# Kernel tuning notes

Measured on AMD Instinct MI355X. Metric: run time of the kernel, lower is better.

The kernel has to match this reference:

```python
import jax, jax.numpy as jnp
import numpy as np

EPS = 1e-6

def _feature_map(x):
    # elu(x) + 1  (positive feature map)
    return jax.nn.elu(x) + 1.0

def setup_inputs() -> dict:
    key = jax.random.key(0)
    k1, k2, k3 = jax.random.split(key, 3)
    B, N, H, D = 4, 4096, 8, 64
    M = 64
    return {
        "queries": jax.random.normal(k1, (B, N, H, D), dtype=jnp.float32),
        "keys": jax.random.normal(k2, (B, N, H, D), dtype=jnp.float32),
        "values": jax.random.normal(k3, (B, N, H, M), dtype=jnp.float32),
        "attn_mask": jnp.zeros((1,), dtype=bool),
    }

def reference(queries, keys, values, attn_mask):
    Q = _feature_map(queries)            # [b,n,h,d]
    K = _feature_map(keys)               # [b,n,h,d]
    KV = jnp.einsum('bnhd,bnhm->bhmd', K, values)          # [b,h,m,d]
    K_sum = K.sum(axis=1)                                  # [b,h,d]
    Z = 1.0 / (jnp.einsum('bnhd,bhd->bnh', Q, K_sum) + EPS)  # [b,n,h]
    V = jnp.einsum('bnhd,bhmd,bnh->bnhm', Q, KV, Z)        # [b,n,h,m]
    return V
```

## Files before the change

kernel.cpp:

```cpp
#include <hip/hip_runtime.h>


#define EPSC 1e-6f

constexpr int Bq = 4;
constexpr int Nq = 4096;
constexpr int Hq = 8;
constexpr int Dq = 64;
constexpr int Mq = 64;
constexpr int BH = Bq * Hq;
constexpr int RSTR = Hq * Dq;
constexpr int TILESZ = Mq * Dq;

__device__ __forceinline__ float fmap(float x) {
    return x > 0.0f ? x + 1.0f : __expf(x);
}

__global__ __launch_bounds__(256)
void phase1_kv(const float* __restrict__ Kp, const float* __restrict__ Vp,
               float* __restrict__ partKV, float* __restrict__ partKS)
{
    const int wid  = threadIdx.x >> 6;
    const int lane = threadIdx.x & 63;
    const int tile = blockIdx.x * 4 + wid;
    const int bh = blockIdx.x >> 4;
    const int ck = blockIdx.x & 15;
    const int b  = bh >> 3;
    const int h  = bh & 7;
    const int dg = lane & 7;
    const int mg = lane >> 3;
    const int n0base = ck * 256 + wid * 64;

    const float* Kb = Kp + (size_t)(b * Nq + n0base) * RSTR + h * Dq;
    const float* Vb = Vp + (size_t)(b * Nq + n0base) * RSTR + h * Dq;

    float acc[8][8];
    #pragma unroll
    for (int i = 0; i < 8; ++i)
        #pragma unroll
        for (int j = 0; j < 8; ++j) acc[i][j] = 0.0f;
    float ksum[8] = {0.f,0.f,0.f,0.f,0.f,0.f,0.f,0.f};

    #pragma unroll 2
    for (int n0 = 0; n0 < 64; n0 += 4) {
        float4 kA[4], kB[4], vA[4], vB[4];
        #pragma unroll
        for (int u = 0; u < 4; ++u) {
            const float* kr = Kb + (size_t)(n0 + u) * RSTR;
            const float* vr = Vb + (size_t)(n0 + u) * RSTR;
            kA[u] = *(const float4*)(kr + dg * 8);
            kB[u] = *(const float4*)(kr + dg * 8 + 4);
            vA[u] = *(const float4*)(vr + mg * 8);
            vB[u] = *(const float4*)(vr + mg * 8 + 4);
        }
        #pragma unroll
        for (int u = 0; u < 4; ++u) {
            float kf[8], vf[8];
            kf[0] = fmap(kA[u].x); kf[1] = fmap(kA[u].y); kf[2] = fmap(kA[u].z); kf[3] = fmap(kA[u].w);
            kf[4] = fmap(kB[u].x); kf[5] = fmap(kB[u].y); kf[6] = fmap(kB[u].z); kf[7] = fmap(kB[u].w);
            vf[0] = vA[u].x; vf[1] = vA[u].y; vf[2] = vA[u].z; vf[3] = vA[u].w;
            vf[4] = vB[u].x; vf[5] = vB[u].y; vf[6] = vB[u].z; vf[7] = vB[u].w;
            #pragma unroll
            for (int mi = 0; mi < 8; ++mi)
                #pragma unroll
                for (int di = 0; di < 8; ++di)
                    acc[mi][di] = fmaf(vf[mi], kf[di], acc[mi][di]);
            if (mg == 0) {
                #pragma unroll
                for (int di = 0; di < 8; ++di) ksum[di] += kf[di];
            }
        }
    }

    float* dst = partKV + (size_t)tile * TILESZ;
    #pragma unroll
    for (int mi = 0; mi < 8; ++mi) {
        const int m = mg * 8 + mi;
        float4 a0 = make_float4(acc[mi][0], acc[mi][1], acc[mi][2], acc[mi][3]);
        float4 a1 = make_float4(acc[mi][4], acc[mi][5], acc[mi][6], acc[mi][7]);
        *(float4*)&dst[m * Dq + dg * 8]     = a0;
        *(float4*)&dst[m * Dq + dg * 8 + 4] = a1;
    }
    if (mg == 0) {
        float* kd = partKS + (size_t)tile * Dq + dg * 8;
        *(float4*)&kd[0] = make_float4(ksum[0], ksum[1], ksum[2], ksum[3]);
        *(float4*)&kd[4] = make_float4(ksum[4], ksum[5], ksum[6], ksum[7]);
    }
}

__global__ __launch_bounds__(256)
void phase1b_reduce(const float* __restrict__ partKV, const float* __restrict__ partKS,
                    float* __restrict__ KV, float* __restrict__ KS)
{
    const int bh = blockIdx.x >> 2;
    const int q  = blockIdx.x & 3;
    const int t  = threadIdx.x;
    const int off = q * 1024 + t * 4;
    const float* src = partKV + (size_t)bh * 64 * TILESZ;

    float4 a = make_float4(0.f, 0.f, 0.f, 0.f);
    #pragma unroll 8
    for (int p = 0; p < 64; ++p) {
        float4 v = *(const float4*)(src + (size_t)p * TILESZ + off);
        a.x += v.x; a.y += v.y; a.z += v.z; a.w += v.w;
    }
    *(float4*)&KV[(size_t)bh * TILESZ + off] = a;

    if (q == 0 && t < Dq) {
        const float* ks = partKS + (size_t)bh * 64 * Dq;
        float s = 0.0f;
        #pragma unroll 8
        for (int p = 0; p < 64; ++p) s += ks[p * Dq + t];
        KS[bh * Dq + t] = s;
    }
}

constexpr int RC2 = 256;

__global__ __launch_bounds__(256, 2)
void phase2_out(const float* __restrict__ Qp, const float* __restrict__ wsKV,
                const float* __restrict__ wsKS, float* __restrict__ Out)
{
    constexpr int CH = Nq / RC2;
    const int bh = blockIdx.x / CH;
    const int ck = blockIdx.x - bh * CH;
    const int b  = bh >> 3;
    const int h  = bh & 7;

    __shared__ float sKV[Mq * 68];
    __shared__ float sKS[Dq];

    const int tid = threadIdx.x;
    const float* kvsrc = wsKV + (size_t)bh * TILESZ;
    #pragma unroll
    for (int it = 0; it < 4; ++it) {
        const int flat = tid * 4 + it * 1024;
        const int m = flat >> 6, d = flat & 63;
        *(float4*)&sKV[m * 68 + d] = *(const float4*)(kvsrc + flat);
    }
    if (tid < 16) {
        *(float4*)&sKS[tid * 4] = *(const float4*)(wsKS + bh * Dq + tid * 4);
    }
    __syncthreads();

    const int mg = tid & 7;
    const int rg = tid >> 3;
    const int row0 = ck * RC2 + rg * 8;
    const float* Qb = Qp + (size_t)(b * Nq + row0) * RSTR + h * Dq;

    float acc[8][8];
    float zac[8];
    #pragma unroll
    for (int i = 0; i < 8; ++i) {
        zac[i] = 0.0f;
        #pragma unroll
        for (int j = 0; j < 8; ++j) acc[i][j] = 0.0f;
    }

    #pragma unroll 2
    for (int d4 = 0; d4 < 16; ++d4) {
        const float4 ks4 = *(const float4*)&sKS[d4 * 4];
        float qf[8][4];
        #pragma unroll
        for (int i = 0; i < 8; ++i) {
            const float4 q = *(const float4*)(Qb + (size_t)i * RSTR + d4 * 4);
            qf[i][0] = fmap(q.x); qf[i][1] = fmap(q.y);
            qf[i][2] = fmap(q.z); qf[i][3] = fmap(q.w);
            zac[i] = fmaf(qf[i][0], ks4.x, zac[i]);
            zac[i] = fmaf(qf[i][1], ks4.y, zac[i]);
            zac[i] = fmaf(qf[i][2], ks4.z, zac[i]);
            zac[i] = fmaf(qf[i][3], ks4.w, zac[i]);
        }
        #pragma unroll
        for (int mi = 0; mi < 8; ++mi) {
            const float4 kv4 = *(const float4*)&sKV[(mg + 8 * mi) * 68 + d4 * 4];
            #pragma unroll
            for (int i = 0; i < 8; ++i) {
                acc[i][mi] = fmaf(qf[i][0], kv4.x, acc[i][mi]);
                acc[i][mi] = fmaf(qf[i][1], kv4.y, acc[i][mi]);
                acc[i][mi] = fmaf(qf[i][2], kv4.z, acc[i][mi]);
                acc[i][mi] = fmaf(qf[i][3], kv4.w, acc[i][mi]);
            }
        }
    }

    float* Ob = Out + (size_t)(b * Nq + row0) * RSTR + h * Mq;
    #pragma unroll
    for (int i = 0; i < 8; ++i) {
        const float z = 1.0f / (zac[i] + EPSC);
        #pragma unroll
        for (int mi = 0; mi < 8; ++mi)
            Ob[(size_t)i * RSTR + mg + 8 * mi] = acc[i][mi] * z;
    }
}

extern "C" void kernel_launch(void* const* d_in, const int* in_sizes, int n_in,
                              void* d_out, int out_size, void* d_ws, size_t ws_size,
                              hipStream_t stream)
{
    (void)in_sizes; (void)n_in; (void)out_size; (void)ws_size;
    const float* Q = (const float*)d_in[0];
    const float* K = (const float*)d_in[1];
    const float* V = (const float*)d_in[2];
    float* out = (float*)d_out;

    float* partKV = out;
    float* wsKV   = (float*)d_ws;
    float* wsKS   = wsKV + (size_t)BH * TILESZ;
    float* partKS = wsKS + (size_t)BH * Dq;

    phase1_kv<<<BH * 16, 256, 0, stream>>>(K, V, partKV, partKS);
    phase1b_reduce<<<BH * 4, 256, 0, stream>>>(partKV, partKS, wsKV, wsKS);
    phase2_out<<<BH * (Nq / RC2), 256, 0, stream>>>(Q, wsKV, wsKS, out);
}
```

Baseline: 243.6 us.

## Restructure all three kernels with new thread mappings and finer partitioning

```diff
diff --git a/kernel.cpp b/kernel.cpp
--- a/kernel.cpp
+++ b/kernel.cpp
@@ -20,177 +20,153 @@
 void phase1_kv(const float* __restrict__ Kp, const float* __restrict__ Vp,
                float* __restrict__ partKV, float* __restrict__ partKS)
 {
-    const int wid  = threadIdx.x >> 6;
+    const int t  = blockIdx.x;
+    const int bh = t >> 6, ck = t & 63;
+    const int b  = bh >> 3, h = bh & 7;
+    const int w    = threadIdx.x >> 6;
     const int lane = threadIdx.x & 63;
-    const int tile = blockIdx.x * 4 + wid;
-    const int bh = blockIdx.x >> 4;
-    const int ck = blockIdx.x & 15;
-    const int b  = bh >> 3;
-    const int h  = bh & 7;
-    const int dg = lane & 7;
-    const int mg = lane >> 3;
-    const int n0base = ck * 256 + wid * 64;
+    const int m0   = w * 16;
 
-    const float* Kb = Kp + (size_t)(b * Nq + n0base) * RSTR + h * Dq;
-    const float* Vb = Vp + (size_t)(b * Nq + n0base) * RSTR + h * Dq;
+    const float* Kb = Kp + ((size_t)(b * Nq + ck * 64) * Hq + h) * Dq;
+    const float* Vb = Vp + ((size_t)(b * Nq + ck * 64) * Hq + h) * Mq;
 
-    float acc[8][8];
+    float acc[16];
     #pragma unroll
-    for (int i = 0; i < 8; ++i)
-        #pragma unroll
-        for (int j = 0; j < 8; ++j) acc[i][j] = 0.0f;
-    float ksum[8] = {0.f,0.f,0.f,0.f,0.f,0.f,0.f,0.f};
+    for (int i = 0; i < 16; ++i) acc[i] = 0.0f;
+    float ksum = 0.0f;
 
     #pragma unroll 2
-    for (int n0 = 0; n0 < 64; n0 += 4) {
-        float4 kA[4], kB[4], vA[4], vB[4];
+    for (int n = 0; n < 64; n += 2) {
+        const float k0 = Kb[(size_t)n * RSTR + lane];
+        const float k1 = Kb[(size_t)(n + 1) * RSTR + lane];
+        const float* v0 = Vb + (size_t)n * RSTR + m0;
+        const float* v1 = Vb + (size_t)(n + 1) * RSTR + m0;
+        float4 va[4], vb[4];
         #pragma unroll
-        for (int u = 0; u < 4; ++u) {
-            const float* kr = Kb + (size_t)(n0 + u) * RSTR;
-            const float* vr = Vb + (size_t)(n0 + u) * RSTR;
-            kA[u] = *(const float4*)(kr + dg * 8);
-            kB[u] = *(const float4*)(kr + dg * 8 + 4);
-            vA[u] = *(const float4*)(vr + mg * 8);
-            vB[u] = *(const float4*)(vr + mg * 8 + 4);
+        for (int j = 0; j < 4; ++j) {
+            va[j] = *(const float4*)(v0 + j * 4);
+            vb[j] = *(const float4*)(v1 + j * 4);
         }
+        const float kf0 = fmap(k0);
+        const float kf1 = fmap(k1);
+        ksum += kf0 + kf1;
         #pragma unroll
-        for (int u = 0; u < 4; ++u) {
-            float kf[8], vf[8];
-            kf[0] = fmap(kA[u].x); kf[1] = fmap(kA[u].y); kf[2] = fmap(kA[u].z); kf[3] = fmap(kA[u].w);
-            kf[4] = fmap(kB[u].x); kf[5] = fmap(kB[u].y); kf[6] = fmap(kB[u].z); kf[7] = fmap(kB[u].w);
-            vf[0] = vA[u].x; vf[1] = vA[u].y; vf[2] = vA[u].z; vf[3] = vA[u].w;
-            vf[4] = vB[u].x; vf[5] = vB[u].y; vf[6] = vB[u].z; vf[7] = vB[u].w;
-            #pragma unroll
-            for (int mi = 0; mi < 8; ++mi)
-                #pragma unroll
-                for (int di = 0; di < 8; ++di)
-                    acc[mi][di] = fmaf(vf[mi], kf[di], acc[mi][di]);
-            if (mg == 0) {
-                #pragma unroll
-                for (int di = 0; di < 8; ++di) ksum[di] += kf[di];
-            }
+        for (int j = 0; j < 4; ++j) {
+            acc[j*4+0] = fmaf(kf0, va[j].x, acc[j*4+0]);
+            acc[j*4+1] = fmaf(kf0, va[j].y, acc[j*4+1]);
+            acc[j*4+2] = fmaf(kf0, va[j].z, acc[j*4+2]);
+            acc[j*4+3] = fmaf(kf0, va[j].w, acc[j*4+3]);
+            acc[j*4+0] = fmaf(kf1, vb[j].x, acc[j*4+0]);
+            acc[j*4+1] = fmaf(kf1, vb[j].y, acc[j*4+1]);
+            acc[j*4+2] = fmaf(kf1, vb[j].z, acc[j*4+2]);
+            acc[j*4+3] = fmaf(kf1, vb[j].w, acc[j*4+3]);
         }
     }
 
-    float* dst = partKV + (size_t)tile * TILESZ;
+    float* dst = partKV + (size_t)t * TILESZ;
     #pragma unroll
-    for (int mi = 0; mi < 8; ++mi) {
-        const int m = mg * 8 + mi;
-        float4 a0 = make_float4(acc[mi][0], acc[mi][1], acc[mi][2], acc[mi][3]);
-        float4 a1 = make_float4(acc[mi][4], acc[mi][5], acc[mi][6], acc[mi][7]);
-        *(float4*)&dst[m * Dq + dg * 8]     = a0;
-        *(float4*)&dst[m * Dq + dg * 8 + 4] = a1;
-    }
-    if (mg == 0) {
-        float* kd = partKS + (size_t)tile * Dq + dg * 8;
-        *(float4*)&kd[0] = make_float4(ksum[0], ksum[1], ksum[2], ksum[3]);
-        *(float4*)&kd[4] = make_float4(ksum[4], ksum[5], ksum[6], ksum[7]);
-    }
+    for (int mi = 0; mi < 16; ++mi)
+        dst[(m0 + mi) * Dq + lane] = acc[mi];
+    if (w == 0)
+        partKS[(size_t)t * Dq + lane] = ksum;
 }
 
 __global__ __launch_bounds__(256)
 void phase1b_reduce(const float* __restrict__ partKV, const float* __restrict__ partKS,
                     float* __restrict__ KV, float* __restrict__ KS)
 {
-    const int bh = blockIdx.x >> 2;
-    const int q  = blockIdx.x & 3;
-    const int t  = threadIdx.x;
-    const int off = q * 1024 + t * 4;
-    const float* src = partKV + (size_t)bh * 64 * TILESZ;
+    const int bh = blockIdx.x >> 4, six = blockIdx.x & 15;
+    const int f  = threadIdx.x & 63, pg = threadIdx.x >> 6;
+    const size_t base = (size_t)bh * 64 * TILESZ + six * 256 + f * 4;
 
     float4 a = make_float4(0.f, 0.f, 0.f, 0.f);
-    #pragma unroll 8
-    for (int p = 0; p < 64; ++p) {
-        float4 v = *(const float4*)(src + (size_t)p * TILESZ + off);
+    #pragma unroll
+    for (int p = 0; p < 16; ++p) {
+        const float4 v = *(const float4*)(partKV + base + (size_t)(pg * 16 + p) * TILESZ);
         a.x += v.x; a.y += v.y; a.z += v.z; a.w += v.w;
     }
-    *(float4*)&KV[(size_t)bh * TILESZ + off] = a;
 
-    if (q == 0 && t < Dq) {
-        const float* ks = partKS + (size_t)bh * 64 * Dq;
-        float s = 0.0f;
-        #pragma unroll 8
-        for (int p = 0; p < 64; ++p) s += ks[p * Dq + t];
-        KS[bh * Dq + t] = s;
+    float ks = 0.0f;
+    if (six == 0) {
+        #pragma unroll
+        for (int p = 0; p < 16; ++p)
+            ks += partKS[(size_t)(bh * 64 + pg * 16 + p) * Dq + f];
+    }
+
+    __shared__ float4 sred[4][64];
+    __shared__ float  sks[4][64];
+    sred[pg][f] = a;
+    sks[pg][f]  = ks;
+    __syncthreads();
+
+    if (pg == 0) {
+        float4 r  = sred[0][f];
+        const float4 r1 = sred[1][f], r2 = sred[2][f], r3 = sred[3][f];
+        r.x += r1.x + r2.x + r3.x;
+        r.y += r1.y + r2.y + r3.y;
+        r.z += r1.z + r2.z + r3.z;
+        r.w += r1.w + r2.w + r3.w;
+        *(float4*)(KV + (size_t)bh * TILESZ + six * 256 + f * 4) = r;
+        if (six == 0)
+            KS[bh * Dq + f] = sks[0][f] + sks[1][f] + sks[2][f] + sks[3][f];
     }
 }
 
-constexpr int RC2 = 256;
+__global__ __launch_bounds__(256)
+void phase2_out(const float* __restrict__ Qp, const float* __restrict__ KV,
+                const float* __restrict__ KS, float* __restrict__ Out)
+{
+    const int blk = blockIdx.x;
+    const int bh = blk >> 5, ck = blk & 31;
+    const int b  = bh >> 3,  h  = bh & 7;
+    const int mg = threadIdx.x & 7;
+    const int rt = threadIdx.x >> 3;
+    const int row0 = ck * 128 + rt * 4;
 
-__global__ __launch_bounds__(256, 2)
-void phase2_out(const float* __restrict__ Qp, const float* __restrict__ wsKV,
-                const float* __restrict__ wsKS, float* __restrict__ Out)
-{
-    constexpr int CH = Nq / RC2;
-    const int bh = blockIdx.x / CH;
-    const int ck = blockIdx.x - bh * CH;
-    const int b  = bh >> 3;
-    const int h  = bh & 7;
+    const float* Qb  = Qp + ((size_t)(b * Nq + row0) * Hq + h) * Dq;
+    const float* KVb = KV + (size_t)bh * TILESZ + mg * 8 * Dq;
+    const float* KSb = KS + bh * Dq;
 
-    __shared__ float sKV[Mq * 68];
-    __shared__ float sKS[Dq];
-
-    const int tid = threadIdx.x;
-    const float* kvsrc = wsKV + (size_t)bh * TILESZ;
+    float acc[4][8];
+    float zac[4] = {0.f, 0.f, 0.f, 0.f};
     #pragma unroll
-    for (int it = 0; it < 4; ++it) {
-        const int flat = tid * 4 + it * 1024;
-        const int m = flat >> 6, d = flat & 63;
-        *(float4*)&sKV[m * 68 + d] = *(const float4*)(kvsrc + flat);
-    }
-    if (tid < 16) {
-        *(float4*)&sKS[tid * 4] = *(const float4*)(wsKS + bh * Dq + tid * 4);
-    }
-    __syncthreads();
-
-    const int mg = tid & 7;
-    const int rg = tid >> 3;
-    const int row0 = ck * RC2 + rg * 8;
-    const float* Qb = Qp + (size_t)(b * Nq + row0) * RSTR + h * Dq;
-
-    float acc[8][8];
-    float zac[8];
-    #pragma unroll
-    for (int i = 0; i < 8; ++i) {
-        zac[i] = 0.0f;
+    for (int i = 0; i < 4; ++i)
         #pragma unroll
         for (int j = 0; j < 8; ++j) acc[i][j] = 0.0f;
-    }
 
-    #pragma unroll 2
+    #pragma unroll 4
     for (int d4 = 0; d4 < 16; ++d4) {
-        const float4 ks4 = *(const float4*)&sKS[d4 * 4];
-        float qf[8][4];
+        const float4 ks4 = *(const float4*)(KSb + d4 * 4);
+        float4 kv[8];
         #pragma unroll
-        for (int i = 0; i < 8; ++i) {
+        for (int mi = 0; mi < 8; ++mi)
+            kv[mi] = *(const float4*)(KVb + mi * Dq + d4 * 4);
+        #pragma unroll
+        for (int i = 0; i < 4; ++i) {
             const float4 q = *(const float4*)(Qb + (size_t)i * RSTR + d4 * 4);
-            qf[i][0] = fmap(q.x); qf[i][1] = fmap(q.y);
-            qf[i][2] = fmap(q.z); qf[i][3] = fmap(q.w);
-            zac[i] = fmaf(qf[i][0], ks4.x, zac[i]);
-            zac[i] = fmaf(qf[i][1], ks4.y, zac[i]);
-            zac[i] = fmaf(qf[i][2], ks4.z, zac[i]);
-            zac[i] = fmaf(qf[i][3], ks4.w, zac[i]);
-        }
-        #pragma unroll
-        for (int mi = 0; mi < 8; ++mi) {
-            const float4 kv4 = *(const float4*)&sKV[(mg + 8 * mi) * 68 + d4 * 4];
+            const float q0 = fmap(q.x), q1 = fmap(q.y), q2 = fmap(q.z), q3 = fmap(q.w);
+            zac[i] = fmaf(q0, ks4.x, zac[i]);
+            zac[i] = fmaf(q1, ks4.y, zac[i]);
+            zac[i] = fmaf(q2, ks4.z, zac[i]);
+            zac[i] = fmaf(q3, ks4.w, zac[i]);
             #pragma unroll
-            for (int i = 0; i < 8; ++i) {
-                acc[i][mi] = fmaf(qf[i][0], kv4.x, acc[i][mi]);
-                acc[i][mi] = fmaf(qf[i][1], kv4.y, acc[i][mi]);
-                acc[i][mi] = fmaf(qf[i][2], kv4.z, acc[i][mi]);
-                acc[i][mi] = fmaf(qf[i][3], kv4.w, acc[i][mi]);
+            for (int mi = 0; mi < 8; ++mi) {
+                acc[i][mi] = fmaf(q0, kv[mi].x, acc[i][mi]);
+                acc[i][mi] = fmaf(q1, kv[mi].y, acc[i][mi]);
+                acc[i][mi] = fmaf(q2, kv[mi].z, acc[i][mi]);
+                acc[i][mi] = fmaf(q3, kv[mi].w, acc[i][mi]);
             }
         }
     }
 
-    float* Ob = Out + (size_t)(b * Nq + row0) * RSTR + h * Mq;
+    float* Ob = Out + ((size_t)(b * Nq + row0) * Hq + h) * Mq + mg * 8;
     #pragma unroll
-    for (int i = 0; i < 8; ++i) {
+    for (int i = 0; i < 4; ++i) {
         const float z = 1.0f / (zac[i] + EPSC);
-        #pragma unroll
-        for (int mi = 0; mi < 8; ++mi)
-            Ob[(size_t)i * RSTR + mg + 8 * mi] = acc[i][mi] * z;
+        const float4 o0 = make_float4(acc[i][0]*z, acc[i][1]*z, acc[i][2]*z, acc[i][3]*z);
+        const float4 o1 = make_float4(acc[i][4]*z, acc[i][5]*z, acc[i][6]*z, acc[i][7]*z);
+        *(float4*)(Ob + (size_t)i * RSTR)     = o0;
+        *(float4*)(Ob + (size_t)i * RSTR + 4) = o1;
     }
 }
 
@@ -209,7 +185,7 @@
     float* wsKS   = wsKV + (size_t)BH * TILESZ;
     float* partKS = wsKS + (size_t)BH * Dq;
 
-    phase1_kv<<<BH * 16, 256, 0, stream>>>(K, V, partKV, partKS);
-    phase1b_reduce<<<BH * 4, 256, 0, stream>>>(partKV, partKS, wsKV, wsKS);
-    phase2_out<<<BH * (Nq / RC2), 256, 0, stream>>>(Q, wsKV, wsKS, out);
+    phase1_kv<<<2048, 256, 0, stream>>>(K, V, partKV, partKS);
+    phase1b_reduce<<<512, 256, 0, stream>>>(partKV, partKS, wsKV, wsKS);
+    phase2_out<<<1024, 256, 0, stream>>>(Q, wsKV, wsKS, out);
 }
```

Result: slower. 280.0 us (+14.9%).
